# Kernel tuning notes

Measured on AMD Instinct MI355X. Metric: run time of the kernel, lower is better.

## Reference

```python
import jax, jax.numpy as jnp
import numpy as np

D_MODEL = 768; D_REF = 768; N_LAYER = 8
EXPAND = 2; D_STATE = 128; HEADDIM = 64; D_CONV = 4
D_INNER = EXPAND * D_MODEL              # 1536
NHEADS = D_INNER // HEADDIM             # 24
CONV_DIM = D_INNER + 2 * D_STATE        # 1792
D_IN_PROJ = 2 * D_INNER + 2 * D_STATE + NHEADS  # 3352
AH = 8; AD = 64; AINNER = AH * AD       # cross-attn heads/dim
RMS_EPS = 1e-5; LN_EPS = 1e-6


def silu(x):
    return x * jax.nn.sigmoid(x)


def rmsnorm(x, w, eps=RMS_EPS):
    x = x.astype(jnp.float32)
    return x * jax.lax.rsqrt(jnp.mean(x * x, axis=-1, keepdims=True) + eps) * w


def ln_noaffine(x, eps=LN_EPS):
    m = jnp.mean(x, -1, keepdims=True)
    v = jnp.mean((x - m) ** 2, -1, keepdims=True)
    return (x - m) * jax.lax.rsqrt(v + eps)


def mamba2_mixer(u, in_w, conv_w, conv_b, dt_bias, A_log, D_ssm, nrm_w, out_w, out_b):
    Bsz, L, _ = u.shape
    zxbcdt = u @ in_w                                        # (B,L,3352)
    z = zxbcdt[..., :D_INNER]
    xBC = zxbcdt[..., D_INNER:D_INNER + CONV_DIM]
    dt = jax.nn.softplus(zxbcdt[..., D_INNER + CONV_DIM:] + dt_bias)  # (B,L,H)
    # causal depthwise conv over sequence + SiLU
    xt = jnp.transpose(xBC, (0, 2, 1))                       # (B,C,L)
    xt = jax.lax.conv_general_dilated(xt, conv_w[:, None, :], (1,), [(D_CONV - 1, 0)],
                                      feature_group_count=CONV_DIM)
    xBC = silu(jnp.transpose(xt, (0, 2, 1)) + conv_b)
    x = xBC[..., :D_INNER].reshape(Bsz, L, NHEADS, HEADDIM)
    Bm = xBC[..., D_INNER:D_INNER + D_STATE]                 # (B,L,N)
    Cm = xBC[..., D_INNER + D_STATE:]                        # (B,L,N)
    dA = jnp.exp(dt * (-jnp.exp(A_log)))                     # (B,L,H)

    def step(h, inp):
        dA_t, dt_t, x_t, B_t, C_t = inp
        dBx = jnp.einsum('bh,bhp,bn->bhpn', dt_t, x_t, B_t)
        h = h * dA_t[:, :, None, None] + dBx                 # (B,H,P,N)
        y = jnp.einsum('bhpn,bn->bhp', h, C_t)
        return h, y

    h0 = jnp.zeros((Bsz, NHEADS, HEADDIM, D_STATE), u.dtype)
    xs = (jnp.moveaxis(dA, 1, 0), jnp.moveaxis(dt, 1, 0), jnp.moveaxis(x, 1, 0),
          jnp.moveaxis(Bm, 1, 0), jnp.moveaxis(Cm, 1, 0))
    _, ys = jax.lax.scan(step, h0, xs)
    y = jnp.moveaxis(ys, 0, 1) + x * D_ssm[None, None, :, None]
    y = y.reshape(Bsz, L, D_INNER)
    y = rmsnorm(y * silu(z), nrm_w)                          # gated RMSNorm (norm_before_gate=False)
    return y @ out_w + out_b


def cross_attention(x, c, q_w, k_w, v_w, o_w, o_b):
    B, L, _ = x.shape
    q = (x @ q_w).reshape(B, L, AH, AD)
    k = (c @ k_w).reshape(B, -1, AH, AD)
    v = (c @ v_w).reshape(B, -1, AH, AD)
    a = jax.nn.softmax(jnp.einsum('blhd,bmhd->bhlm', q, k) * (AD ** -0.5), axis=-1)
    o = jnp.einsum('bhlm,bmhd->blhd', a, v).reshape(B, L, AINNER)
    return o @ o_w + o_b


def block_fwd(hidden, residual, cond, p):
    residual = hidden + residual
    hidden = rmsnorm(residual, p['norm_w'])
    aff = silu(jnp.mean(cond, axis=1)) @ p['ada_w'] + p['ada_b']
    sh_mba, sc_mba, g_mba, sh_msa, sc_msa, g_msa = jnp.split(aff, 6, axis=-1)
    mod = lambda t, sh, sc: t * (1 + sc[:, None, :]) + sh[:, None, :]
    hidden = hidden + g_mba[:, None, :] * mamba2_mixer(
        mod(hidden, sh_mba, sc_mba), p['in_w'], p['conv_w'], p['conv_b'],
        p['dt_bias'], p['A_log'], p['D_ssm'], p['ssm_norm_w'], p['out_w'], p['out_b'])
    hidden = hidden + g_msa[:, None, :] * cross_attention(
        mod(ln_noaffine(hidden), sh_msa, sc_msa), cond,
        p['q_w'], p['k_w'], p['v_w'], p['o_w'], p['o_b'])
    return hidden, residual


def backbone(hidden_states, ref_embeddings, norm_w, ada_w, ada_b, in_w, conv_w, conv_b,
             dt_bias, A_log, D_ssm, ssm_norm_w, out_w, out_b,
             q_w, k_w, v_w, o_w, o_b, norm_f_w):
    params = dict(norm_w=norm_w, ada_w=ada_w, ada_b=ada_b, in_w=in_w, conv_w=conv_w,
                  conv_b=conv_b, dt_bias=dt_bias, A_log=A_log, D_ssm=D_ssm,
                  ssm_norm_w=ssm_norm_w, out_w=out_w, out_b=out_b,
                  q_w=q_w, k_w=k_w, v_w=v_w, o_w=o_w, o_b=o_b)

    @jax.checkpoint
    def body(carry, lp):
        h, r = carry
        h, r = block_fwd(h, r, ref_embeddings, lp)
        return (h, r), None

    carry0 = (hidden_states, jnp.zeros_like(hidden_states))
    (h, r), _ = jax.lax.scan(body, carry0, params)
    return rmsnorm(h + r, norm_f_w)


def setup_inputs() -> dict:
    key = jax.random.key(0)
    ks = jax.random.split(key, 16)
    B, L, LC = 2, 512, 64

    def w(k, shape, s=0.02):
        return jax.random.normal(k, shape, jnp.float32) * s

    return dict(
        hidden_states=jax.random.normal(ks[0], (B, L, D_MODEL), jnp.float32),
        ref_embeddings=jax.random.normal(ks[1], (B, LC, D_REF), jnp.float32),
        norm_w=jnp.ones((N_LAYER, D_MODEL), jnp.float32),
        ada_w=w(ks[2], (N_LAYER, D_REF, 6 * D_MODEL)),
        ada_b=jnp.zeros((N_LAYER, 6 * D_MODEL), jnp.float32),
        in_w=w(ks[3], (N_LAYER, D_MODEL, D_IN_PROJ)),
        conv_w=w(ks[4], (N_LAYER, CONV_DIM, D_CONV), 0.2),
        conv_b=jnp.zeros((N_LAYER, CONV_DIM), jnp.float32),
        dt_bias=jnp.log(jnp.expm1(jax.random.uniform(ks[5], (N_LAYER, NHEADS), jnp.float32, 1e-3, 0.1))),
        A_log=jnp.log(jax.random.uniform(ks[6], (N_LAYER, NHEADS), jnp.float32, 1.0, 16.0)),
        D_ssm=jnp.ones((N_LAYER, NHEADS), jnp.float32),
        ssm_norm_w=jnp.ones((N_LAYER, D_INNER), jnp.float32),
        out_w=w(ks[7], (N_LAYER, D_INNER, D_MODEL)),
        out_b=jnp.zeros((N_LAYER, D_MODEL), jnp.float32),
        q_w=w(ks[8], (N_LAYER, D_MODEL, AINNER)),
        k_w=w(ks[9], (N_LAYER, D_REF, AINNER)),
        v_w=w(ks[10], (N_LAYER, D_REF, AINNER)),
        o_w=w(ks[11], (N_LAYER, AINNER, D_MODEL)),
        o_b=jnp.zeros((N_LAYER, D_MODEL), jnp.float32),
        norm_f_w=jnp.ones((D_MODEL,), jnp.float32),
    )


def reference(hidden_states, ref_embeddings, norm_w, ada_w, ada_b, in_w, conv_w, conv_b,
              dt_bias, A_log, D_ssm, ssm_norm_w, out_w, out_b,
              q_w, k_w, v_w, o_w, o_b, norm_f_w):
    return backbone(hidden_states, ref_embeddings, norm_w, ada_w, ada_b, in_w, conv_w,
                    conv_b, dt_bias, A_log, D_ssm, ssm_norm_w, out_w, out_b,
                    q_w, k_w, v_w, o_w, o_b, norm_f_w)
```

## Files before the change

### kernel.cpp

```cpp
#include <hip/hip_runtime.h>
#include <hip/hip_bf16.h>
#include <math.h>

#define D_MODEL   768
#define N_LAYER   8
#define D_INNER   1536
#define D_STATE   128
#define HEADDIM   64
#define NHEADS    24
#define CONV_DIM  1792
#define D_IN_PROJ 3352
#define AH        8
#define AD        64
#define AINNER    512
#define BSZ       2
#define SEQ       512
#define LC        64
#define ROWS      (BSZ*SEQ)
#define NCHUNK    8
#define CT        64
#define NP1       3456
#define AFF       4608

typedef __attribute__((ext_vector_type(8))) short bf16x8;
typedef __attribute__((ext_vector_type(4))) float f32x4;
typedef __attribute__((ext_vector_type(8))) unsigned short u16x8;

__device__ __forceinline__ float siluf(float x) { return x / (1.f + expf(-x)); }

__device__ __forceinline__ unsigned short f2b(float x) {
    __hip_bfloat16 h = __float2bfloat16(x);
    return __builtin_bit_cast(unsigned short, h);
}
__device__ __forceinline__ float b2f(unsigned short u) {
    unsigned v = ((unsigned)u) << 16;
    return __builtin_bit_cast(float, v);
}

__device__ __forceinline__ void gload16(const void* g, void* l) {
    __builtin_amdgcn_global_load_lds(
        (const __attribute__((address_space(1))) unsigned int*)g,
        (__attribute__((address_space(3))) unsigned int*)l,
        16, 0, 0);
}

__device__ __forceinline__ float block_sum_256(float v, float* s4) {
    #pragma unroll
    for (int o = 32; o > 0; o >>= 1) v += __shfl_down(v, o, 64);
    __syncthreads();
    if ((threadIdx.x & 63) == 0) s4[threadIdx.x >> 6] = v;
    __syncthreads();
    return s4[0] + s4[1] + s4[2] + s4[3];
}

__global__ void k_prep(const float* __restrict__ ref_emb, unsigned short* __restrict__ ref_bf,
                       float* __restrict__ smc, const float* __restrict__ adab,
                       float* __restrict__ aff_all,
                       const float* __restrict__ in_w, const float* __restrict__ out_w,
                       const float* __restrict__ qw, const float* __restrict__ kw,
                       const float* __restrict__ vw, const float* __restrict__ ow,
                       unsigned short* __restrict__ in_wt, unsigned short* __restrict__ out_wt,
                       unsigned short* __restrict__ qwt, unsigned short* __restrict__ kwt,
                       unsigned short* __restrict__ vwt, unsigned short* __restrict__ owt) {
    int blk = blockIdx.x, t = threadIdx.x;
    if (blk < 96) {
        int i4 = blk * 256 + t;
        float4 v = *(const float4*)&ref_emb[(size_t)i4 * 4];
        ushort4 o; o.x = f2b(v.x); o.y = f2b(v.y); o.z = f2b(v.z); o.w = f2b(v.w);
        *(ushort4*)&ref_bf[(size_t)i4 * 4] = o;
        return;
    }
    if (blk < 102) {
        int i = (blk - 96) * 256 + t;
        if (i < BSZ * D_MODEL) {
            int b = i / D_MODEL, d = i % D_MODEL;
            const float* p = ref_emb + (size_t)b * LC * D_MODEL + d;
            float s = 0.f;
            #pragma unroll 4
            for (int l = 0; l < LC; l++) s += p[l * D_MODEL];
            smc[i] = siluf(s * (1.f / (float)LC));
        }
        return;
    }
    if (blk < 390) {
        int i = (blk - 102) * 256 + t;
        int j = i % AFF; int l = (i / AFF) >> 1;
        aff_all[i] = adab[l * AFF + j];
        return;
    }
    const float* src; unsigned short* dst; int K, N, n0, k0;
    int u = blk - 390;
    if (u < 2592) {
        int z = u / 324, rem = u % 324;
        k0 = (rem / 27) * 64; n0 = (rem % 27) * 128;
        src = in_w + (size_t)z * 768 * 3352; dst = in_wt + (size_t)z * 3456 * 768;
        K = 768; N = 3352;
    } else if (u < 3744) {
        u -= 2592; int z = u / 144, rem = u % 144;
        k0 = (rem / 6) * 64; n0 = (rem % 6) * 128;
        src = out_w + (size_t)z * 1536 * 768; dst = out_wt + (size_t)z * 768 * 1536;
        K = 1536; N = 768;
    } else if (u < 4896) {
        u -= 3744; int z = u / 48, rem = u % 48;
        k0 = (rem / 4) * 64; n0 = (rem % 4) * 128;
        int which = z >> 3, layer = z & 7;
        src = (which == 0 ? qw : which == 1 ? kw : vw) + (size_t)layer * 768 * 512;
        dst = (which == 0 ? qwt : which == 1 ? kwt : vwt) + (size_t)layer * 512 * 768;
        K = 768; N = 512;
    } else {
        u -= 4896; int z = u / 48, rem = u % 48;
        k0 = (rem / 6) * 64; n0 = (rem % 6) * 128;
        src = ow + (size_t)z * 512 * 768; dst = owt + (size_t)z * 768 * 512;
        K = 512; N = 768;
    }
    __shared__ float tile[64][129];
    #pragma unroll
    for (int p = 0; p < 8; p++) {
        int idx = p * 256 + t;
        int k = idx >> 5, cg = idx & 31;
        int n = n0 + cg * 4;
        float4 v = (float4){0.f, 0.f, 0.f, 0.f};
        if (n < N) v = *(const float4*)&src[(size_t)(k0 + k) * N + n];
        tile[k][cg * 4 + 0] = v.x; tile[k][cg * 4 + 1] = v.y;
        tile[k][cg * 4 + 2] = v.z; tile[k][cg * 4 + 3] = v.w;
    }
    __syncthreads();
    #pragma unroll
    for (int p = 0; p < 4; p++) {
        int idx = p * 256 + t;
        int n = idx >> 3, kk = (idx & 7) * 8;
        u16x8 o;
        #pragma unroll
        for (int e = 0; e < 8; e++) o[e] = f2b(tile[kk + e][n]);
        *(u16x8*)&dst[(size_t)(n0 + n) * K + k0 + kk] = o;
    }
}

__global__ __launch_bounds__(256)
void k_kvada(const unsigned short* __restrict__ A, const unsigned short* __restrict__ Kwt,
             const unsigned short* __restrict__ Vwt, unsigned short* __restrict__ Kb,
             unsigned short* __restrict__ Vb,
             const float* __restrict__ smc, const float* __restrict__ adaw,
             float* __restrict__ aff_all) {
    int z = blockIdx.z;
    if (z >= 16) {
        int zz = z - 16; int l = zz >> 3, kc = zz & 7;
        int j = blockIdx.x * 256 + threadIdx.x;
        const float* w = adaw + (size_t)l * D_MODEL * AFF + j;
        const float* x0 = smc;
        const float* x1 = smc + D_MODEL;
        float s0 = 0.f, s1 = 0.f;
        int d0 = kc * 96;
        #pragma unroll 8
        for (int d = d0; d < d0 + 96; d++) {
            float wv = w[(size_t)d * AFF];
            s0 += x0[d] * wv; s1 += x1[d] * wv;
        }
        atomicAdd(&aff_all[(size_t)l * BSZ * AFF + j], s0);
        atomicAdd(&aff_all[(size_t)l * BSZ * AFF + AFF + j], s1);
        return;
    }
    if (blockIdx.x >= 4) return;
    int layer = z >> 1; int which = z & 1;
    const unsigned short* Bt = (which ? Vwt : Kwt) + (size_t)layer * AINNER * D_MODEL;
    unsigned short* C = (which ? Vb : Kb) + (size_t)layer * (BSZ * LC) * AINNER;
    __shared__ __align__(16) unsigned short As[128][32];
    __shared__ __align__(16) unsigned short Bs[128][32];
    int n0 = blockIdx.x * 128;
    int tid = threadIdx.x;
    int lane = tid & 63, wave = tid >> 6;
    int wm = (wave >> 1) * 64, wn = (wave & 1) * 64;
    int l15 = lane & 15, quad = lane >> 4;
    f32x4 acc[4][4];
    #pragma unroll
    for (int i = 0; i < 4; i++)
        #pragma unroll
        for (int j = 0; j < 4; j++) acc[i][j] = (f32x4){0.f, 0.f, 0.f, 0.f};
    int srow = tid >> 2, schunk = (tid & 3) * 8;
    for (int k0 = 0; k0 < D_MODEL; k0 += 32) {
        #pragma unroll
        for (int ps = 0; ps < 2; ps++) {
            int r = srow + ps * 64;
            gload16(&A[(size_t)r * D_MODEL + k0 + schunk], &As[r][schunk]);
            gload16(&Bt[(size_t)(n0 + r) * D_MODEL + k0 + schunk], &Bs[r][schunk]);
        }
        __syncthreads();
        bf16x8 af[4], bfr[4];
        #pragma unroll
        for (int i = 0; i < 4; i++) af[i]  = *(const bf16x8*)&As[wm + i * 16 + l15][quad * 8];
        #pragma unroll
        for (int j = 0; j < 4; j++) bfr[j] = *(const bf16x8*)&Bs[wn + j * 16 + l15][quad * 8];
        #pragma unroll
        for (int i = 0; i < 4; i++)
            #pragma unroll
            for (int j = 0; j < 4; j++)
                acc[i][j] = __builtin_amdgcn_mfma_f32_16x16x32_bf16(af[i], bfr[j], acc[i][j], 0, 0, 0);
        __syncthreads();
    }
    #pragma unroll
    for (int i = 0; i < 4; i++) {
        #pragma unroll
        for (int j = 0; j < 4; j++) {
            int col = n0 + wn + j * 16 + l15;
            #pragma unroll
            for (int r = 0; r < 4; r++) {
                int row = wm + i * 16 + quad * 4 + r;
                C[(size_t)row * AINNER + col] = f2b(acc[i][j][r]);
            }
        }
    }
}

__global__ __launch_bounds__(256)
void k_gemm_sk(const unsigned short* __restrict__ A, const unsigned short* __restrict__ Bt,
               float* __restrict__ C, int M, int N, int K, int Kc) {
    int z = blockIdx.z;
    C += (size_t)z * M * N;
    int kbeg = z * Kc;
    int kend = kbeg + Kc; if (kend > K) kend = K;
    int nt = (kend - kbeg) >> 5;
    __shared__ __align__(16) unsigned short As[2][128][32];
    __shared__ __align__(16) unsigned short Bs[2][128][32];
    int m0 = blockIdx.y * 128, n0 = blockIdx.x * 128;
    int tid = threadIdx.x;
    int lane = tid & 63, wave = tid >> 6;
    int wm = (wave >> 1) * 64, wn = (wave & 1) * 64;
    int l15 = lane & 15, quad = lane >> 4;
    f32x4 acc[4][4];
    #pragma unroll
    for (int i = 0; i < 4; i++)
        #pragma unroll
        for (int j = 0; j < 4; j++) acc[i][j] = (f32x4){0.f, 0.f, 0.f, 0.f};

    int srow = tid >> 2;
    int schunk = (tid & 3) * 8;

    #define STAGE_SK(buf, kk0)                                                        \
        do {                                                                          \
            _Pragma("unroll")                                                         \
            for (int ps = 0; ps < 2; ps++) {                                          \
                int r = srow + ps * 64;                                               \
                gload16(&A[(size_t)(m0 + r) * K + (kk0) + schunk], &As[buf][r][schunk]); \
                gload16(&Bt[(size_t)(n0 + r) * K + (kk0) + schunk], &Bs[buf][r][schunk]); \
            }                                                                         \
        } while (0)

    STAGE_SK(0, kbeg);
    int cur = 0;
    for (int it = 0; it < nt; ++it) {
        if (it + 1 < nt) {
            STAGE_SK(cur ^ 1, kbeg + (it + 1) * 32);
            asm volatile("s_waitcnt vmcnt(4)" ::: "memory");
        } else {
            asm volatile("s_waitcnt vmcnt(0)" ::: "memory");
        }
        __builtin_amdgcn_s_barrier();
        bf16x8 af[4], bfr[4];
        #pragma unroll
        for (int i = 0; i < 4; i++) af[i]  = *(const bf16x8*)&As[cur][wm + i * 16 + l15][quad * 8];
        #pragma unroll
        for (int j = 0; j < 4; j++) bfr[j] = *(const bf16x8*)&Bs[cur][wn + j * 16 + l15][quad * 8];
        #pragma unroll
        for (int i = 0; i < 4; i++)
            #pragma unroll
            for (int j = 0; j < 4; j++)
                acc[i][j] = __builtin_amdgcn_mfma_f32_16x16x32_bf16(af[i], bfr[j], acc[i][j], 0, 0, 0);
        __builtin_amdgcn_s_barrier();
        cur ^= 1;
    }
    #undef STAGE_SK
    #pragma unroll
    for (int i = 0; i < 4; i++) {
        #pragma unroll
        for (int j = 0; j < 4; j++) {
            int col = n0 + wn + j * 16 + l15;
            if (col < N) {
                #pragma unroll
                for (int r = 0; r < 4; r++) {
                    int row = m0 + wm + i * 16 + quad * 4 + r;
                    C[(size_t)row * N + col] = acc[i][j][r];
                }
            }
        }
    }
}

__global__ void k_addrmsmod(const float* __restrict__ hin, const float* __restrict__ raw,
                            const float* __restrict__ bias, const float* __restrict__ affprev,
                            float* __restrict__ residual, const float* __restrict__ normw,
                            const float* __restrict__ affcur,
                            float* __restrict__ hidden_n, unsigned short* __restrict__ u,
                            int has_raw) {
    __shared__ float s4[4];
    const size_t PSTR = (size_t)ROWS * D_MODEL;
    int row = blockIdx.x;
    int b = row >> 9;
    const float* hp = hin + (size_t)row * D_MODEL;
    float* rp = residual + (size_t)row * D_MODEL;
    float v[3]; float ss = 0.f;
    #pragma unroll
    for (int j = 0; j < 3; j++) {
        int d = threadIdx.x + j * 256;
        float x = hp[d];
        if (has_raw) {
            float g = affprev[b * AFF + 3840 + d];
            float rawv = raw[(size_t)row * D_MODEL + d] + raw[PSTR + (size_t)row * D_MODEL + d];
            x += g * (rawv + bias[d]) + rp[d];
        }
        rp[d] = x; v[j] = x; ss += x * x;
    }
    ss = block_sum_256(ss, s4);
    float inv = rsqrtf(ss / (float)D_MODEL + 1e-5f);
    const float* sh = affcur + b * AFF;
    const float* sc = affcur + b * AFF + 768;
    #pragma unroll
    for (int j = 0; j < 3; j++) {
        int d = threadIdx.x + j * 256;
        float hn = v[j] * inv * normw[d];
        hidden_n[(size_t)row * D_MODEL + d] = hn;
        u[(size_t)row * D_MODEL + d] = f2b(hn * (1.f + sc[d]) + sh[d]);
    }
}

__global__ void k_convdt(const float* __restrict__ zx, const float* __restrict__ convw,
                         const float* __restrict__ convb, const float* __restrict__ dtbias,
                         unsigned short* __restrict__ xBC, float* __restrict__ dtb) {
    const size_t PSTRZ = (size_t)ROWS * D_IN_PROJ;
    int blk = blockIdx.x, tid = threadIdx.x;
    if (blk >= 448) {
        int i = (blk - 448) * 256 + tid;
        int h = i % NHEADS; int row = i / NHEADS;
        size_t off = (size_t)row * D_IN_PROJ + D_INNER + CONV_DIM + h;
        float x = zx[off] + zx[off + PSTRZ] + dtbias[h];
        dtb[i] = (x > 20.f) ? x : log1pf(expf(x));
        return;
    }
    int g = blk * 256 + tid;
    int cg = g % 448, rg = g / 448;
    int c0 = cg * 4, row0 = rg * 4;
    int l0 = row0 & 511;
    size_t rowbase = (size_t)row0 * D_IN_PROJ + D_INNER + c0;
    float rr[7][4];
    #pragma unroll
    for (int k = 0; k < 7; k++) {
        int tpos = l0 - 3 + k;
        if (tpos >= 0) {
            size_t idx = rowbase + (size_t)(k - 3) * D_IN_PROJ;
            float4 a = *(const float4*)&zx[idx];
            float4 b4 = *(const float4*)&zx[idx + PSTRZ];
            rr[k][0] = a.x + b4.x; rr[k][1] = a.y + b4.y;
            rr[k][2] = a.z + b4.z; rr[k][3] = a.w + b4.w;
        } else {
            rr[k][0] = rr[k][1] = rr[k][2] = rr[k][3] = 0.f;
        }
    }
    float4 w0 = *(const float4*)&convw[(size_t)c0 * 4];
    float4 w1 = *(const float4*)&convw[(size_t)(c0 + 1) * 4];
    float4 w2 = *(const float4*)&convw[(size_t)(c0 + 2) * 4];
    float4 w3 = *(const float4*)&convw[(size_t)(c0 + 3) * 4];
    float4 bb = *(const float4*)&convb[c0];
    #pragma unroll
    for (int r = 0; r < 4; r++) {
        ushort4 o;
        float a0 = bb.x + w0.x * rr[r][0] + w0.y * rr[r + 1][0] + w0.z * rr[r + 2][0] + w0.w * rr[r + 3][0];
        float a1 = bb.y + w1.x * rr[r][1] + w1.y * rr[r + 1][1] + w1.z * rr[r + 2][1] + w1.w * rr[r + 3][1];
        float a2 = bb.z + w2.x * rr[r][2] + w2.y * rr[r + 1][2] + w2.z * rr[r + 2][2] + w2.w * rr[r + 3][2];
        float a3 = bb.w + w3.x * rr[r][3] + w3.y * rr[r + 1][3] + w3.z * rr[r + 2][3] + w3.w * rr[r + 3][3];
        o.x = f2b(siluf(a0)); o.y = f2b(siluf(a1));
        o.z = f2b(siluf(a2)); o.w = f2b(siluf(a3));
        *(ushort4*)&xBC[(size_t)(row0 + r) * CONV_DIM + c0] = o;
    }
}

__global__ __launch_bounds__(256)
void k_ssm_par(const unsigned short* __restrict__ xBC, const float* __restrict__ dtb,
               const float* __restrict__ Alog, const float* __restrict__ Dssm,
               float* __restrict__ y, unsigned short* __restrict__ Sbuf,
               float* __restrict__ Pbuf) {
    __shared__ unsigned short sB[64][136];
    __shared__ unsigned short sC[64][136];
    __shared__ unsigned short sXT[64][72];
    __shared__ unsigned short sG[64][72];
    __shared__ unsigned short sBT[128][72];
    __shared__ float sL[64], sDt[64];
    int c = blockIdx.x, bh = blockIdx.y;
    int h = bh % NHEADS, b = bh / NHEADS;
    int tid = threadIdx.x;
    int lane = tid & 63, wave = tid >> 6;
    int l15 = lane & 15, quad = lane >> 4;
    int r = tid >> 2, q4 = tid & 3;
    int base = b * SEQ + c * CT;
    float a_h = expf(Alog[h]);
    float Dh = Dssm[h];
    if (tid < 64) {
        float dt = dtb[(base + tid) * NHEADS + h];
        float v = -a_h * dt;
        #pragma unroll
        for (int off = 1; off < 64; off <<= 1) {
            float u2 = __shfl_up(v, off, 64);
            if (tid >= off) v += u2;
        }
        sL[tid] = v; sDt[tid] = dt;
    }
    const unsigned short* xrow = xBC + (size_t)(base + r) * CONV_DIM;
    #pragma unroll
    for (int j = 0; j < 4; j++) {
        int n0 = q4 * 32 + j * 8;
        uint4 v = *(const uint4*)&xrow[D_INNER + n0];
        *(uint4*)&sB[r][n0] = v;
        const unsigned short* hv = (const unsigned short*)&v;
        #pragma unroll
        for (int e = 0; e < 8; e++) sBT[n0 + e][r] = hv[e];
        uint4 w = *(const uint4*)&xrow[D_INNER + D_STATE + n0];
        *(uint4*)&sC[r][n0] = w;
    }
    #pragma unroll
    for (int j = 0; j < 2; j++) {
        int p0 = q4 * 16 + j * 8;
        uint4 v = *(const uint4*)&xrow[h * HEADDIM + p0];
        const unsigned short* hv = (const unsigned short*)&v;
        #pragma unroll
        for (int e = 0; e < 8; e++) sXT[p0 + e][r] = hv[e];
    }
    __syncthreads();
    if (tid == 0) Pbuf[bh * NCHUNK + c] = expf(sL[63]);

    f32x4 acc1[4];
    #pragma unroll
    for (int j = 0; j < 4; j++) acc1[j] = (f32x4){0.f, 0.f, 0.f, 0.f};
    #pragma unroll
    for (int k0 = 0; k0 < 4; k0++) {
        bf16x8 a = *(const bf16x8*)&sC[wave * 16 + l15][k0 * 32 + quad * 8];
        #pragma unroll
        for (int nt = 0; nt < 4; nt++) {
            bf16x8 bv = *(const bf16x8*)&sB[nt * 16 + l15][k0 * 32 + quad * 8];
            acc1[nt] = __builtin_amdgcn_mfma_f32_16x16x32_bf16(a, bv, acc1[nt], 0, 0, 0);
        }
    }
    #pragma unroll
    for (int nt = 0; nt < 4; nt++) {
        int s = nt * 16 + l15;
        float Ls = sL[s], dts = sDt[s];
        #pragma unroll
        for (int rr = 0; rr < 4; rr++) {
            int i = wave * 16 + quad * 4 + rr;
            float g = (s <= i) ? acc1[nt][rr] * expf(sL[i] - Ls) * dts : 0.f;
            sG[i][s] = f2b(g);
        }
    }
    __syncthreads();

    f32x4 acc2[4];
    #pragma unroll
    for (int j = 0; j < 4; j++) acc2[j] = (f32x4){0.f, 0.f, 0.f, 0.f};
    #pragma unroll
    for (int k0 = 0; k0 < 2; k0++) {
        bf16x8 a = *(const bf16x8*)&sG[wave * 16 + l15][k0 * 32 + quad * 8];
        #pragma unroll
        for (int nt = 0; nt < 4; nt++) {
            bf16x8 bv = *(const bf16x8*)&sXT[nt * 16 + l15][k0 * 32 + quad * 8];
            acc2[nt] = __builtin_amdgcn_mfma_f32_16x16x32_bf16(a, bv, acc2[nt], 0, 0, 0);
        }
    }
    #pragma unroll
    for (int nt = 0; nt < 4; nt++) {
        int p = nt * 16 + l15;
        #pragma unroll
        for (int rr = 0; rr < 4; rr++) {
            int i = wave * 16 + quad * 4 + rr;
            float xv = b2f(sXT[p][i]);
            y[(size_t)(base + i) * D_INNER + h * HEADDIM + p] = acc2[nt][rr] + Dh * xv;
        }
    }
    __syncthreads();
    {
        float wr2 = expf(sL[63] - sL[r]) * sDt[r];
        #pragma unroll
        for (int j = 0; j < 16; j++) {
            int pp = q4 * 16 + j;
            sG[pp][r] = f2b(b2f(sXT[pp][r]) * wr2);
        }
    }
    __syncthreads();
    f32x4 accS[8];
    #pragma unroll
    for (int j = 0; j < 8; j++) accS[j] = (f32x4){0.f, 0.f, 0.f, 0.f};
    #pragma unroll
    for (int k0 = 0; k0 < 2; k0++) {
        bf16x8 a = *(const bf16x8*)&sG[wave * 16 + l15][k0 * 32 + quad * 8];
        #pragma unroll
        for (int nt = 0; nt < 8; nt++) {
            bf16x8 bv = *(const bf16x8*)&sBT[nt * 16 + l15][k0 * 32 + quad * 8];
            accS[nt] = __builtin_amdgcn_mfma_f32_16x16x32_bf16(a, bv, accS[nt], 0, 0, 0);
        }
    }
    unsigned short* sout = Sbuf + ((size_t)bh * NCHUNK + c) * 8192;
    #pragma unroll
    for (int nt = 0; nt < 8; nt++) {
        int n = nt * 16 + l15;
        #pragma unroll
        for (int rr = 0; rr < 4; rr++) {
            int p = wave * 16 + quad * 4 + rr;
            sout[p * 128 + n] = f2b(accS[nt][rr]);
        }
    }
}

__global__ __launch_bounds__(256)
void k_ssm_fix(const unsigned short* __restrict__ xBC, const float* __restrict__ dtb,
               const float* __restrict__ Alog, const unsigned short* __restrict__ Sbuf,
               const float* __restrict__ Pbuf, float* __restrict__ y) {
    __shared__ unsigned short sC[64][136];
    __shared__ unsigned short sHB[64][136];
    __shared__ float sL[64];
    int c = blockIdx.x + 1, bh = blockIdx.y;
    int h = bh % NHEADS, b = bh / NHEADS;
    int tid = threadIdx.x;
    int lane = tid & 63, wave = tid >> 6;
    int l15 = lane & 15, quad = lane >> 4;
    int r = tid >> 2, q4 = tid & 3;
    int base = b * SEQ + c * CT;
    if (tid < 64) {
        float dt = dtb[(base + tid) * NHEADS + h];
        float v = -expf(Alog[h]) * dt;
        #pragma unroll
        for (int off = 1; off < 64; off <<= 1) {
            float u2 = __shfl_up(v, off, 64);
            if (tid >= off) v += u2;
        }
        sL[tid] = v;
    }
    float hacc[32];
    #pragma unroll
    for (int e = 0; e < 32; e++) hacc[e] = 0.f;
    {
        const unsigned short* sp = Sbuf + (size_t)bh * NCHUNK * 8192 + r * 128 + q4 * 32;
        float w = 1.f;
        for (int j = c - 1; j >= 0; j--) {
            const unsigned short* srow = sp + (size_t)j * 8192;
            #pragma unroll
            for (int q = 0; q < 4; q++) {
                bf16x8 vv = *(const bf16x8*)&srow[q * 8];
                #pragma unroll
                for (int e = 0; e < 8; e++)
                    hacc[q * 8 + e] += w * b2f((unsigned short)vv[e]);
            }
            w *= Pbuf[bh * NCHUNK + j];
        }
    }
    __syncthreads();
    #pragma unroll
    for (int e = 0; e < 32; e++) sHB[r][q4 * 32 + e] = f2b(hacc[e]);
    {
        float el = expf(sL[r]);
        const unsigned short* xrow = xBC + (size_t)(base + r) * CONV_DIM + D_INNER + D_STATE;
        #pragma unroll
        for (int j = 0; j < 4; j++) {
            int n0 = q4 * 32 + j * 8;
            uint4 v = *(const uint4*)&xrow[n0];
            const unsigned short* hv = (const unsigned short*)&v;
            #pragma unroll
            for (int e = 0; e < 8; e++) sC[r][n0 + e] = f2b(b2f(hv[e]) * el);
        }
    }
    __syncthreads();
    f32x4 acc[4];
    #pragma unroll
    for (int j = 0; j < 4; j++) acc[j] = (f32x4){0.f, 0.f, 0.f, 0.f};
    #pragma unroll
    for (int k0 = 0; k0 < 4; k0++) {
        bf16x8 a = *(const bf16x8*)&sC[wave * 16 + l15][k0 * 32 + quad * 8];
        #pragma unroll
        for (int nt = 0; nt < 4; nt++) {
            bf16x8 bv = *(const bf16x8*)&sHB[nt * 16 + l15][k0 * 32 + quad * 8];
            acc[nt] = __builtin_amdgcn_mfma_f32_16x16x32_bf16(a, bv, acc[nt], 0, 0, 0);
        }
    }
    #pragma unroll
    for (int nt = 0; nt < 4; nt++) {
        int p = nt * 16 + l15;
        #pragma unroll
        for (int rr = 0; rr < 4; rr++) {
            int i = wave * 16 + quad * 4 + rr;
            size_t idx = (size_t)(base + i) * D_INNER + h * HEADDIM + p;
            y[idx] += acc[nt][rr];
        }
    }
}

__global__ void k_gatednorm(const float* __restrict__ yscan, const float* __restrict__ zx,
                            const float* __restrict__ nw, unsigned short* __restrict__ out) {
    __shared__ float s4[4];
    const size_t PSTRZ = (size_t)ROWS * D_IN_PROJ;
    int row = blockIdx.x;
    const float* yp = yscan + (size_t)row * D_INNER;
    const float* zp0 = zx + (size_t)row * D_IN_PROJ;
    const float* zp1 = zp0 + PSTRZ;
    float v[6]; float ss = 0.f;
    #pragma unroll
    for (int j = 0; j < 6; j++) {
        int d = threadIdx.x + j * 256;
        float val = yp[d] * siluf(zp0[d] + zp1[d]);
        v[j] = val; ss += val * val;
    }
    ss = block_sum_256(ss, s4);
    float inv = rsqrtf(ss / (float)D_INNER + 1e-5f);
    #pragma unroll
    for (int j = 0; j < 6; j++) {
        int d = threadIdx.x + j * 256;
        out[(size_t)row * D_INNER + d] = f2b(v[j] * inv * nw[d]);
    }
}

__global__ void k_fuse_ln(const float* __restrict__ hidden_n, const float* __restrict__ tmp,
                          const float* __restrict__ outb, const float* __restrict__ aff,
                          float* __restrict__ hidden2, unsigned short* __restrict__ attnx) {
    __shared__ float s4[4];
    const size_t PSTR = (size_t)ROWS * D_MODEL;
    int row = blockIdx.x;
    int b = row >> 9;
    const float* gm = aff + b * AFF + 1536;
    float v[3]; float s = 0.f;
    #pragma unroll
    for (int j = 0; j < 3; j++) {
        int d = threadIdx.x + j * 256;
        size_t idx = (size_t)row * D_MODEL + d;
        float t = tmp[idx] + tmp[idx + PSTR] + tmp[idx + 2 * PSTR] + tmp[idx + 3 * PSTR];
        float x = hidden_n[idx] + gm[d] * (t + outb[d]);
        hidden2[idx] = x;
        v[j] = x; s += x;
    }
    float mean = block_sum_256(s, s4) / (float)D_MODEL;
    float ss = 0.f;
    #pragma unroll
    for (int j = 0; j < 3; j++) { float c = v[j] - mean; ss += c * c; }
    float var = block_sum_256(ss, s4) / (float)D_MODEL;
    float inv = rsqrtf(var + 1e-6f);
    const float* sh = aff + b * AFF + 2304;
    const float* sc = aff + b * AFF + 3072;
    #pragma unroll
    for (int j = 0; j < 3; j++) {
        int d = threadIdx.x + j * 256;
        float xh = (v[j] - mean) * inv;
        attnx[(size_t)row * D_MODEL + d] = f2b(xh * (1.f + sc[d]) + sh[d]);
    }
}

__global__ __launch_bounds__(256)
void k_attn(const unsigned short* __restrict__ attnx, const unsigned short* __restrict__ qwt,
            const unsigned short* __restrict__ kb, const unsigned short* __restrict__ vb,
            unsigned short* __restrict__ ob) {
    int blk = blockIdx.x;
    int lt = blk & 15; int h = (blk >> 4) & 7; int b = blk >> 7;
    __shared__ unsigned short sK[64][72];
    __shared__ unsigned short sVT[64][72];
    __shared__ unsigned short sA[32][136];
    __shared__ unsigned short sW[64][136];
    __shared__ unsigned short sQb[32][72];
    __shared__ unsigned short sP[32][72];
    int tid = threadIdx.x;
    {
        int r = tid >> 2, c0 = (tid & 3) * 16;
        const unsigned short* kp = kb + (size_t)(b * LC + r) * AINNER + h * AD + c0;
        const unsigned short* vp = vb + (size_t)(b * LC + r) * AINNER + h * AD + c0;
        #pragma unroll
        for (int j = 0; j < 4; j++) {
            *(ushort4*)&sK[r][c0 + j * 4] = *(const ushort4*)&kp[j * 4];
            ushort4 vv = *(const ushort4*)&vp[j * 4];
            const unsigned short* hv = (const unsigned short*)&vv;
            #pragma unroll
            for (int e = 0; e < 4; e++) sVT[c0 + j * 4 + e][r] = hv[e];
        }
    }
    int lane = tid & 63, wave = tid >> 6;
    int l15 = lane & 15, quad = lane >> 4;
    int rt = wave >> 1, cp = (wave & 1) * 2;
    f32x4 accq[2];
    accq[0] = (f32x4){0.f, 0.f, 0.f, 0.f};
    accq[1] = (f32x4){0.f, 0.f, 0.f, 0.f};
    const size_t arow_base = (size_t)(b * SEQ + lt * 32) * D_MODEL;
    for (int k0 = 0; k0 < D_MODEL; k0 += 128) {
        __syncthreads();
        #pragma unroll
        for (int j = 0; j < 2; j++) {
            int s = tid + j * 256; int row = s >> 4, c8 = (s & 15) * 8;
            *(uint4*)&sA[row][c8] =
                *(const uint4*)&attnx[arow_base + (size_t)row * D_MODEL + k0 + c8];
        }
        #pragma unroll
        for (int j = 0; j < 4; j++) {
            int s = tid + j * 256; int row = s >> 4, c8 = (s & 15) * 8;
            *(uint4*)&sW[row][c8] =
                *(const uint4*)&qwt[(size_t)(h * AD + row) * D_MODEL + k0 + c8];
        }
        __syncthreads();
        #pragma unroll
        for (int ks = 0; ks < 4; ks++) {
            bf16x8 af = *(const bf16x8*)&sA[rt * 16 + l15][ks * 32 + quad * 8];
            #pragma unroll
            for (int j = 0; j < 2; j++) {
                bf16x8 bf = *(const bf16x8*)&sW[(cp + j) * 16 + l15][ks * 32 + quad * 8];
                accq[j] = __builtin_amdgcn_mfma_f32_16x16x32_bf16(af, bf, accq[j], 0, 0, 0);
            }
        }
    }
    #pragma unroll
    for (int j = 0; j < 2; j++)
        #pragma unroll
        for (int rr = 0; rr < 4; rr++)
            sQb[rt * 16 + quad * 4 + rr][(cp + j) * 16 + l15] = f2b(accq[j][rr] * 0.125f);
    __syncthreads();
    if (wave < 2) {
        int qt = wave;
        f32x4 s[4];
        #pragma unroll
        for (int mt = 0; mt < 4; mt++) s[mt] = (f32x4){0.f, 0.f, 0.f, 0.f};
        #pragma unroll
        for (int k0 = 0; k0 < 2; k0++) {
            bf16x8 aq = *(const bf16x8*)&sQb[qt * 16 + l15][k0 * 32 + quad * 8];
            #pragma unroll
            for (int mt = 0; mt < 4; mt++) {
                bf16x8 bk = *(const bf16x8*)&sK[mt * 16 + l15][k0 * 32 + quad * 8];
                s[mt] = __builtin_amdgcn_mfma_f32_16x16x32_bf16(aq, bk, s[mt], 0, 0, 0);
            }
        }
        #pragma unroll
        for (int rr = 0; rr < 4; rr++) {
            float mx = fmaxf(fmaxf(s[0][rr], s[1][rr]), fmaxf(s[2][rr], s[3][rr]));
            #pragma unroll
            for (int off = 8; off > 0; off >>= 1) mx = fmaxf(mx, __shfl_xor(mx, off, 64));
            float e0 = expf(s[0][rr] - mx), e1 = expf(s[1][rr] - mx);
            float e2 = expf(s[2][rr] - mx), e3 = expf(s[3][rr] - mx);
            float sum = e0 + e1 + e2 + e3;
            #pragma unroll
            for (int off = 8; off > 0; off >>= 1) sum += __shfl_xor(sum, off, 64);
            float inv = 1.f / sum;
            int q = qt * 16 + quad * 4 + rr;
            sP[q][0 * 16 + l15] = f2b(e0 * inv);
            sP[q][1 * 16 + l15] = f2b(e1 * inv);
            sP[q][2 * 16 + l15] = f2b(e2 * inv);
            sP[q][3 * 16 + l15] = f2b(e3 * inv);
        }
    }
    __syncthreads();
    {
        int qt = wave >> 1, dp = (wave & 1) * 2;
        f32x4 o[2];
        o[0] = (f32x4){0.f, 0.f, 0.f, 0.f};
        o[1] = (f32x4){0.f, 0.f, 0.f, 0.f};
        #pragma unroll
        for (int k0 = 0; k0 < 2; k0++) {
            bf16x8 ap = *(const bf16x8*)&sP[qt * 16 + l15][k0 * 32 + quad * 8];
            #pragma unroll
            for (int j = 0; j < 2; j++) {
                bf16x8 bv = *(const bf16x8*)&sVT[(dp + j) * 16 + l15][k0 * 32 + quad * 8];
                o[j] = __builtin_amdgcn_mfma_f32_16x16x32_bf16(ap, bv, o[j], 0, 0, 0);
            }
        }
        #pragma unroll
        for (int j = 0; j < 2; j++) {
            int d = (dp + j) * 16 + l15;
            #pragma unroll
            for (int rr = 0; rr < 4; rr++) {
                int q = qt * 16 + quad * 4 + rr;
                ob[(size_t)(b * SEQ + lt * 32 + q) * AINNER + h * AD + d] = f2b(o[j][rr]);
            }
        }
    }
}

__global__ void k_final(const float* __restrict__ hidden2, const float* __restrict__ raw,
                        const float* __restrict__ bias, const float* __restrict__ aff,
                        const float* __restrict__ residual, const float* __restrict__ w,
                        float* __restrict__ out) {
    __shared__ float s4[4];
    const size_t PSTR = (size_t)ROWS * D_MODEL;
    int row = blockIdx.x;
    int b = row >> 9;
    const float* gm = aff + b * AFF + 3840;
    float v[3]; float ss = 0.f;
    #pragma unroll
    for (int j = 0; j < 3; j++) {
        int d = threadIdx.x + j * 256;
        size_t idx = (size_t)row * D_MODEL + d;
        float rawv = raw[idx] + raw[idx + PSTR];
        float x = hidden2[idx] + gm[d] * (rawv + bias[d]) + residual[idx];
        v[j] = x; ss += x * x;
    }
    ss = block_sum_256(ss, s4);
    float inv = rsqrtf(ss / (float)D_MODEL + 1e-5f);
    #pragma unroll
    for (int j = 0; j < 3; j++) {
        int d = threadIdx.x + j * 256;
        out[(size_t)row * D_MODEL + d] = v[j] * inv * w[d];
    }
}

extern "C" void kernel_launch(void* const* d_in, const int* in_sizes, int n_in,
                              void* d_out, int out_size, void* d_ws, size_t ws_size,
                              hipStream_t stream) {
    const float* hidden_states = (const float*)d_in[0];
    const float* ref_emb  = (const float*)d_in[1];
    const float* norm_w   = (const float*)d_in[2];
    const float* ada_w    = (const float*)d_in[3];
    const float* ada_b    = (const float*)d_in[4];
    const float* in_w     = (const float*)d_in[5];
    const float* conv_w   = (const float*)d_in[6];
    const float* conv_b   = (const float*)d_in[7];
    const float* dt_bias  = (const float*)d_in[8];
    const float* A_log    = (const float*)d_in[9];
    const float* D_ssm    = (const float*)d_in[10];
    const float* ssm_nw   = (const float*)d_in[11];
    const float* out_w    = (const float*)d_in[12];
    const float* out_b    = (const float*)d_in[13];
    const float* q_w      = (const float*)d_in[14];
    const float* k_w      = (const float*)d_in[15];
    const float* v_w      = (const float*)d_in[16];
    const float* o_w      = (const float*)d_in[17];
    const float* o_b      = (const float*)d_in[18];
    const float* norm_f_w = (const float*)d_in[19];
    float* out = (float*)d_out;

    char* p = (char*)d_ws;
    auto alloc = [&](size_t bytes) -> char* {
        char* r = p; p += (bytes + 255) & ~(size_t)255; return r;
    };
    float* residual = (float*)alloc((size_t)ROWS * D_MODEL * 4);
    float* hidden2  = (float*)alloc((size_t)ROWS * D_MODEL * 4);
    float* hidden_n = (float*)alloc((size_t)ROWS * D_MODEL * 4);
    float* tmpM     = (float*)alloc((size_t)4 * ROWS * D_MODEL * 4);
    float* tmpO     = (float*)alloc((size_t)2 * ROWS * D_MODEL * 4);
    float* zx       = (float*)alloc((size_t)2 * ROWS * D_IN_PROJ * 4);
    float* dtb      = (float*)alloc((size_t)ROWS * NHEADS * 4);
    float* yscan    = (float*)alloc((size_t)ROWS * D_INNER * 4);
    float* aff_all  = (float*)alloc((size_t)N_LAYER * BSZ * AFF * 4);
    float* smc      = (float*)alloc((size_t)BSZ * D_MODEL * 4);
    float* Pbuf     = (float*)alloc((size_t)BSZ * NHEADS * NCHUNK * 4);
    unsigned short* xBC    = (unsigned short*)alloc((size_t)ROWS * CONV_DIM * 2);
    unsigned short* Sbuf   = (unsigned short*)alloc((size_t)BSZ * NHEADS * NCHUNK * 8192 * 2);
    unsigned short* u_bf   = (unsigned short*)alloc((size_t)ROWS * D_MODEL * 2);
    unsigned short* ynorm  = (unsigned short*)alloc((size_t)ROWS * D_INNER * 2);
    unsigned short* attnx  = (unsigned short*)alloc((size_t)ROWS * D_MODEL * 2);
    unsigned short* ob     = (unsigned short*)alloc((size_t)ROWS * AINNER * 2);
    unsigned short* ref_bf = (unsigned short*)alloc((size_t)BSZ * LC * D_MODEL * 2);
    unsigned short* kb_all  = (unsigned short*)alloc((size_t)N_LAYER * BSZ * LC * AINNER * 2);
    unsigned short* vb_all  = (unsigned short*)alloc((size_t)N_LAYER * BSZ * LC * AINNER * 2);
    unsigned short* in_wt_all  = (unsigned short*)alloc((size_t)N_LAYER * NP1 * D_MODEL * 2);
    unsigned short* out_wt_all = (unsigned short*)alloc((size_t)N_LAYER * D_MODEL * D_INNER * 2);
    unsigned short* q_wt_all   = (unsigned short*)alloc((size_t)N_LAYER * AINNER * D_MODEL * 2);
    unsigned short* o_wt_all   = (unsigned short*)alloc((size_t)N_LAYER * D_MODEL * AINNER * 2);
    unsigned short* kwt_all = (unsigned short*)alloc((size_t)N_LAYER * AINNER * D_MODEL * 2);
    unsigned short* vwt_all = (unsigned short*)alloc((size_t)N_LAYER * AINNER * D_MODEL * 2);

    k_prep<<<5670, 256, 0, stream>>>(ref_emb, ref_bf, smc, ada_b, aff_all,
                                     in_w, out_w, q_w, k_w, v_w, o_w,
                                     in_wt_all, out_wt_all, q_wt_all, kwt_all, vwt_all,
                                     o_wt_all);
    k_kvada<<<dim3(18, 1, 80), 256, 0, stream>>>(ref_bf, kwt_all, vwt_all, kb_all, vb_all,
                                                 smc, ada_w, aff_all);

    for (int layer = 0; layer < N_LAYER; layer++) {
        const float* L_norm_w  = norm_w  + layer * D_MODEL;
        const float* L_conv_w  = conv_w  + layer * CONV_DIM * 4;
        const float* L_conv_b  = conv_b  + layer * CONV_DIM;
        const float* L_dt_bias = dt_bias + layer * NHEADS;
        const float* L_A_log   = A_log   + layer * NHEADS;
        const float* L_D_ssm   = D_ssm   + layer * NHEADS;
        const float* L_ssm_nw  = ssm_nw  + layer * D_INNER;
        const float* L_out_b   = out_b   + layer * D_MODEL;
        const float* L_o_b_prev= o_b     + (layer - 1) * D_MODEL;
        const float* L_aff     = aff_all + (size_t)layer * BSZ * AFF;
        const float* L_aff_prev= aff_all + (size_t)(layer - 1) * BSZ * AFF;
        const unsigned short* in_wt  = in_wt_all  + (size_t)layer * NP1 * D_MODEL;
        const unsigned short* out_wt = out_wt_all + (size_t)layer * D_MODEL * D_INNER;
        const unsigned short* q_wt   = q_wt_all   + (size_t)layer * AINNER * D_MODEL;
        const unsigned short* o_wt   = o_wt_all   + (size_t)layer * D_MODEL * AINNER;

        k_addrmsmod<<<ROWS, 256, 0, stream>>>(
            layer == 0 ? hidden_states : hidden2, tmpO,
            layer == 0 ? o_b : L_o_b_prev,
            layer == 0 ? aff_all : L_aff_prev,
            residual, L_norm_w, L_aff, hidden_n, u_bf, layer == 0 ? 0 : 1);
        k_gemm_sk<<<dim3(NP1 / 128, ROWS / 128, 2), 256, 0, stream>>>(u_bf, in_wt, zx, ROWS, D_IN_PROJ, D_MODEL, 384);
        k_convdt<<<544, 256, 0, stream>>>(zx, L_conv_w, L_conv_b, L_dt_bias, xBC, dtb);
        k_ssm_par<<<dim3(NCHUNK, BSZ * NHEADS), 256, 0, stream>>>(xBC, dtb, L_A_log, L_D_ssm, yscan, Sbuf, Pbuf);
        k_ssm_fix<<<dim3(NCHUNK - 1, BSZ * NHEADS), 256, 0, stream>>>(xBC, dtb, L_A_log, Sbuf, Pbuf, yscan);
        k_gatednorm<<<ROWS, 256, 0, stream>>>(yscan, zx, L_ssm_nw, ynorm);
        k_gemm_sk<<<dim3(D_MODEL / 128, ROWS / 128, 4), 256, 0, stream>>>(ynorm, out_wt, tmpM, ROWS, D_MODEL, D_INNER, 384);
        k_fuse_ln<<<ROWS, 256, 0, stream>>>(hidden_n, tmpM, L_out_b, L_aff, hidden2, attnx);
        k_attn<<<BSZ * AH * 16, 256, 0, stream>>>(
            attnx, q_wt,
            kb_all + (size_t)layer * BSZ * LC * AINNER,
            vb_all + (size_t)layer * BSZ * LC * AINNER, ob);
        k_gemm_sk<<<dim3(D_MODEL / 128, ROWS / 128, 2), 256, 0, stream>>>(ob, o_wt, tmpO, ROWS, D_MODEL, AINNER, 256);
    }
    k_final<<<ROWS, 256, 0, stream>>>(hidden2, tmpO, o_b + (N_LAYER - 1) * D_MODEL,
                                      aff_all + (size_t)(N_LAYER - 1) * BSZ * AFF,
                                      residual, norm_f_w, out);
}
```

Measured before the change: 1.048 ms.

## Smaller prep transpose tiles, XCD-aware GEMM block swizzle, 4-way split-K for o-proj

The prep kernel's weight transpose now uses 64x64 tiles (about twice as many blocks) and converts ref embeddings 8 floats per thread. The split-K GEMM remaps its flat block index so that consecutive tiles land on the same XCD, aiming for better L2 locality. The attention output projection moves from 2-way to 4-way split-K, and the add/norm and final kernels now sum four partial buffers. This trades more partial-sum traffic and more small blocks for higher occupancy and better cache behaviour.

```diff
diff --git a/kernel.cpp b/kernel.cpp
--- a/kernel.cpp
+++ b/kernel.cpp
@@ -63,15 +63,18 @@
                        unsigned short* __restrict__ qwt, unsigned short* __restrict__ kwt,
                        unsigned short* __restrict__ vwt, unsigned short* __restrict__ owt) {
     int blk = blockIdx.x, t = threadIdx.x;
-    if (blk < 96) {
-        int i4 = blk * 256 + t;
-        float4 v = *(const float4*)&ref_emb[(size_t)i4 * 4];
-        ushort4 o; o.x = f2b(v.x); o.y = f2b(v.y); o.z = f2b(v.z); o.w = f2b(v.w);
-        *(ushort4*)&ref_bf[(size_t)i4 * 4] = o;
+    if (blk < 48) {
+        int i8 = blk * 256 + t;
+        float4 a = *(const float4*)&ref_emb[(size_t)i8 * 8];
+        float4 b4 = *(const float4*)&ref_emb[(size_t)i8 * 8 + 4];
+        u16x8 o;
+        o[0] = f2b(a.x); o[1] = f2b(a.y); o[2] = f2b(a.z); o[3] = f2b(a.w);
+        o[4] = f2b(b4.x); o[5] = f2b(b4.y); o[6] = f2b(b4.z); o[7] = f2b(b4.w);
+        *(u16x8*)&ref_bf[(size_t)i8 * 8] = o;
         return;
     }
-    if (blk < 102) {
-        int i = (blk - 96) * 256 + t;
+    if (blk < 54) {
+        int i = (blk - 48) * 256 + t;
         if (i < BSZ * D_MODEL) {
             int b = i / D_MODEL, d = i % D_MODEL;
             const float* p = ref_emb + (size_t)b * LC * D_MODEL + d;
@@ -82,42 +85,42 @@
         }
         return;
     }
-    if (blk < 390) {
-        int i = (blk - 102) * 256 + t;
+    if (blk < 342) {
+        int i = (blk - 54) * 256 + t;
         int j = i % AFF; int l = (i / AFF) >> 1;
         aff_all[i] = adab[l * AFF + j];
         return;
     }
     const float* src; unsigned short* dst; int K, N, n0, k0;
-    int u = blk - 390;
-    if (u < 2592) {
-        int z = u / 324, rem = u % 324;
-        k0 = (rem / 27) * 64; n0 = (rem % 27) * 128;
+    int u = blk - 342;
+    if (u < 5088) {
+        int z = u / 636, rem = u % 636;
+        k0 = (rem / 53) * 64; n0 = (rem % 53) * 64;
         src = in_w + (size_t)z * 768 * 3352; dst = in_wt + (size_t)z * 3456 * 768;
         K = 768; N = 3352;
-    } else if (u < 3744) {
-        u -= 2592; int z = u / 144, rem = u % 144;
-        k0 = (rem / 6) * 64; n0 = (rem % 6) * 128;
+    } else if (u < 7392) {
+        u -= 5088; int z = u / 288, rem = u % 288;
+        k0 = (rem / 12) * 64; n0 = (rem % 12) * 64;
         src = out_w + (size_t)z * 1536 * 768; dst = out_wt + (size_t)z * 768 * 1536;
         K = 1536; N = 768;
-    } else if (u < 4896) {
-        u -= 3744; int z = u / 48, rem = u % 48;
-        k0 = (rem / 4) * 64; n0 = (rem % 4) * 128;
+    } else if (u < 9696) {
+        u -= 7392; int z = u / 96, rem = u % 96;
+        k0 = (rem / 8) * 64; n0 = (rem % 8) * 64;
         int which = z >> 3, layer = z & 7;
         src = (which == 0 ? qw : which == 1 ? kw : vw) + (size_t)layer * 768 * 512;
         dst = (which == 0 ? qwt : which == 1 ? kwt : vwt) + (size_t)layer * 512 * 768;
         K = 768; N = 512;
     } else {
-        u -= 4896; int z = u / 48, rem = u % 48;
-        k0 = (rem / 6) * 64; n0 = (rem % 6) * 128;
+        u -= 9696; int z = u / 96, rem = u % 96;
+        k0 = (rem / 12) * 64; n0 = (rem % 12) * 64;
         src = ow + (size_t)z * 512 * 768; dst = owt + (size_t)z * 768 * 512;
         K = 512; N = 768;
     }
-    __shared__ float tile[64][129];
-    #pragma unroll
-    for (int p = 0; p < 8; p++) {
-        int idx = p * 256 + t;
-        int k = idx >> 5, cg = idx & 31;
+    __shared__ float tile[64][65];
+    #pragma unroll
+    for (int p2 = 0; p2 < 4; p2++) {
+        int idx = p2 * 256 + t;
+        int k = idx >> 4, cg = idx & 15;
         int n = n0 + cg * 4;
         float4 v = (float4){0.f, 0.f, 0.f, 0.f};
         if (n < N) v = *(const float4*)&src[(size_t)(k0 + k) * N + n];
@@ -126,8 +129,8 @@
     }
     __syncthreads();
     #pragma unroll
-    for (int p = 0; p < 4; p++) {
-        int idx = p * 256 + t;
+    for (int p2 = 0; p2 < 2; p2++) {
+        int idx = p2 * 256 + t;
         int n = idx >> 3, kk = (idx & 7) * 8;
         u16x8 o;
         #pragma unroll
@@ -214,14 +217,21 @@
 __global__ __launch_bounds__(256)
 void k_gemm_sk(const unsigned short* __restrict__ A, const unsigned short* __restrict__ Bt,
                float* __restrict__ C, int M, int N, int K, int Kc) {
-    int z = blockIdx.z;
-    C += (size_t)z * M * N;
-    int kbeg = z * Kc;
+    int gx = gridDim.x, gy = gridDim.y;
+    int nwg = gx * gy * gridDim.z;
+    int flat = (blockIdx.z * gy + blockIdx.y) * gx + blockIdx.x;
+    int q = nwg >> 3, r8 = nwg & 7;
+    int xcd = flat & 7, idx8 = flat >> 3;
+    int swz = (xcd < r8 ? xcd * (q + 1) : r8 * (q + 1) + (xcd - r8) * q) + idx8;
+    int bx = swz % gx; int t2 = swz / gx; int by = t2 % gy; int bz = t2 / gy;
+
+    C += (size_t)bz * M * N;
+    int kbeg = bz * Kc;
     int kend = kbeg + Kc; if (kend > K) kend = K;
     int nt = (kend - kbeg) >> 5;
     __shared__ __align__(16) unsigned short As[2][128][32];
     __shared__ __align__(16) unsigned short Bs[2][128][32];
-    int m0 = blockIdx.y * 128, n0 = blockIdx.x * 128;
+    int m0 = by * 128, n0 = bx * 128;
     int tid = threadIdx.x;
     int lane = tid & 63, wave = tid >> 6;
     int wm = (wave >> 1) * 64, wn = (wave & 1) * 64;
@@ -304,7 +314,8 @@
         float x = hp[d];
         if (has_raw) {
             float g = affprev[b * AFF + 3840 + d];
-            float rawv = raw[(size_t)row * D_MODEL + d] + raw[PSTR + (size_t)row * D_MODEL + d];
+            size_t idx = (size_t)row * D_MODEL + d;
+            float rawv = raw[idx] + raw[idx + PSTR] + raw[idx + 2 * PSTR] + raw[idx + 3 * PSTR];
             x += g * (rawv + bias[d]) + rp[d];
         }
         rp[d] = x; v[j] = x; ss += x * x;
@@ -783,7 +794,7 @@
     for (int j = 0; j < 3; j++) {
         int d = threadIdx.x + j * 256;
         size_t idx = (size_t)row * D_MODEL + d;
-        float rawv = raw[idx] + raw[idx + PSTR];
+        float rawv = raw[idx] + raw[idx + PSTR] + raw[idx + 2 * PSTR] + raw[idx + 3 * PSTR];
         float x = hidden2[idx] + gm[d] * (rawv + bias[d]) + residual[idx];
         v[j] = x; ss += x * x;
     }
@@ -829,7 +840,7 @@
     float* hidden2  = (float*)alloc((size_t)ROWS * D_MODEL * 4);
     float* hidden_n = (float*)alloc((size_t)ROWS * D_MODEL * 4);
     float* tmpM     = (float*)alloc((size_t)4 * ROWS * D_MODEL * 4);
-    float* tmpO     = (float*)alloc((size_t)2 * ROWS * D_MODEL * 4);
+    float* tmpO     = (float*)alloc((size_t)4 * ROWS * D_MODEL * 4);
     float* zx       = (float*)alloc((size_t)2 * ROWS * D_IN_PROJ * 4);
     float* dtb      = (float*)alloc((size_t)ROWS * NHEADS * 4);
     float* yscan    = (float*)alloc((size_t)ROWS * D_INNER * 4);
@@ -852,10 +863,10 @@
     unsigned short* kwt_all = (unsigned short*)alloc((size_t)N_LAYER * AINNER * D_MODEL * 2);
     unsigned short* vwt_all = (unsigned short*)alloc((size_t)N_LAYER * AINNER * D_MODEL * 2);
 
-    k_prep<<<5670, 256, 0, stream>>>(ref_emb, ref_bf, smc, ada_b, aff_all,
-                                     in_w, out_w, q_w, k_w, v_w, o_w,
-                                     in_wt_all, out_wt_all, q_wt_all, kwt_all, vwt_all,
-                                     o_wt_all);
+    k_prep<<<10806, 256, 0, stream>>>(ref_emb, ref_bf, smc, ada_b, aff_all,
+                                      in_w, out_w, q_w, k_w, v_w, o_w,
+                                      in_wt_all, out_wt_all, q_wt_all, kwt_all, vwt_all,
+                                      o_wt_all);
     k_kvada<<<dim3(18, 1, 80), 256, 0, stream>>>(ref_bf, kwt_all, vwt_all, kb_all, vb_all,
                                                  smc, ada_w, aff_all);
 
@@ -892,7 +903,7 @@
             attnx, q_wt,
             kb_all + (size_t)layer * BSZ * LC * AINNER,
             vb_all + (size_t)layer * BSZ * LC * AINNER, ob);
-        k_gemm_sk<<<dim3(D_MODEL / 128, ROWS / 128, 2), 256, 0, stream>>>(ob, o_wt, tmpO, ROWS, D_MODEL, AINNER, 256);
+        k_gemm_sk<<<dim3(D_MODEL / 128, ROWS / 128, 4), 256, 0, stream>>>(ob, o_wt, tmpO, ROWS, D_MODEL, AINNER, 128);
     }
     k_final<<<ROWS, 256, 0, stream>>>(hidden2, tmpO, o_b + (N_LAYER - 1) * D_MODEL,
                                       aff_all + (size_t)(N_LAYER - 1) * BSZ * AFF,
```

Result: no change. 1.034 ms (-1.4%).
